# Kernel tuning notes

Measured on AMD Instinct MI355X. Metric: run time of the kernel, lower is better.

The kernel has to match this reference:

```python
import jax, jax.numpy as jnp
import numpy as np

T, G, D = 64, 1024, 128      # timesteps, detections per timestep, feature dim
N = T * G                    # total points; output rows = 3 + D = 131 cols


def setup_inputs() -> dict:
    key = jax.random.key(0)
    k1, k2 = jax.random.split(key)
    # time column: T distinct timestamps, G detections each (already time-sorted)
    times = jnp.repeat(jnp.arange(T, dtype=jnp.float32), G)
    xy = jax.random.uniform(k1, (N, 2), dtype=jnp.float32) * 128.0
    coor = jnp.concatenate([times[:, None], xy], axis=1)          # [N, 3]
    features = jax.random.normal(k2, (N, D), dtype=jnp.float32)   # [N, 128]
    return {"coor": coor, "features": features, "min_length": 8}


def _traverse(nxt):
    """Greedy chain building with a visited set (faithful to the torch loop).
    nxt[i] = precomputed best cosine match of point i in the next time group
    (-1 if i is in the last group). Returns (out_nodes, cid, clen):
      out_nodes[p] = node emitted at output slot p (all N slots filled),
      cid[p]       = chain id of slot p,
      clen[c]      = length of chain c.
    """
    def chain_cond(carry):
        visited, out, cid, p, cur, length, c = carry
        nx = nxt[cur]
        return (nx >= 0) & (~visited[nx])

    def chain_body(carry):
        visited, out, cid, p, cur, length, c = carry
        nx = nxt[cur]
        visited = visited.at[nx].set(True)
        out = out.at[p].set(nx)
        cid = cid.at[p].set(c)
        return (visited, out, cid, p + 1, nx, length + 1, c)

    def start_chain(st, start):
        visited, out, cid, clen, p, c = st
        visited = visited.at[start].set(True)
        out = out.at[p].set(start)
        cid = cid.at[p].set(c)
        carry = (visited, out, cid, p + 1, start, jnp.int32(1), c)
        visited, out, cid, p, cur, length, _ = jax.lax.while_loop(
            chain_cond, chain_body, carry)
        clen = clen.at[c].set(length)
        return (visited, out, cid, clen, p, c + 1)

    def body(start, st):
        start = jnp.int32(start)
        return jax.lax.cond(st[0][start], lambda s: s,
                            lambda s: start_chain(s, start), st)

    init = (jnp.zeros(N, bool),
            jnp.full(N, -1, jnp.int32),
            jnp.zeros(N, jnp.int32),
            jnp.zeros(N, jnp.int32),
            jnp.int32(0), jnp.int32(0))
    visited, out, cid, clen, p, c = jax.lax.fori_loop(0, N, body, init)
    return out, cid, clen


def reference(coor, features, min_length):
    # sort all points by time (stable; input is already time-sorted)
    order = jnp.argsort(coor[:, 0], stable=True)
    coor = coor[order]
    features = features[order]

    # --- vectorized precompute of the greedy next-match graph ---
    # group points by timestamp: [T, G, D]
    f = features.reshape(T, G, D)
    fn = f / jnp.maximum(jnp.linalg.norm(f, axis=-1, keepdims=True), 1e-6)
    # cosine sims between each time group and the next one: [T-1, G, G]
    sims = jnp.einsum('tgd,thd->tgh', fn[:-1], fn[1:])
    best = jnp.argmax(sims, axis=-1).astype(jnp.int32)        # [T-1, G]
    nxt = jnp.concatenate([
        (jnp.arange(1, T, dtype=jnp.int32)[:, None] * G + best).reshape(-1),
        jnp.full((G,), -1, jnp.int32)])                        # [N]
    nxt = jax.lax.stop_gradient(nxt)

    # --- sequential greedy traversal with visited set ---
    out_nodes, cid, clen = _traverse(nxt)

    # rows = [coor || features] in trajectory order
    rows = jnp.concatenate([coor, features], axis=1)[out_nodes]  # [N, 3+D]
    keep = clen[cid] >= min_length
    # pack kept rows to the top (order preserved), zero-pad the rest
    perm = jnp.argsort(~keep, stable=True)
    return jnp.where(keep[perm][:, None], rows[perm], 0.0)       # [N, 131]
```

## Files before the change

### kernel.cpp

```cpp
#include <hip/hip_runtime.h>
#include <hip/hip_bf16.h>
#include <hip/hip_fp16.h>

#define TT 64
#define GN 1024
#define DK 128
#define NN (TT * GN)
#define OUTC 131
#define TAU 5e-3f
#define CHUNK 64

typedef _Float16 f16x8 __attribute__((ext_vector_type(8)));
typedef float    f32x4 __attribute__((ext_vector_type(4)));

__device__ __forceinline__ unsigned f2h(float f) {
    return (unsigned)__half_as_ushort(__float2half(f));
}

__device__ __forceinline__ void gload_lds16(const void* g, void* l) {
    __builtin_amdgcn_global_load_lds(
        (const __attribute__((address_space(1))) unsigned int*)g,
        (__attribute__((address_space(3))) unsigned int*)l, 16, 0, 0);
}

__global__ void kconv(const float* __restrict__ feat, unsigned* __restrict__ fh,
                      float* __restrict__ rnf, double* __restrict__ rnd,
                      int* __restrict__ rcnt, int* __restrict__ clen) {
    if (blockIdx.x == 0 && threadIdx.x < 63) rcnt[threadIdx.x] = 0;
    if (blockIdx.x < 256) clen[blockIdx.x * 256 + threadIdx.x] = 0;
    int row  = blockIdx.x * 4 + (threadIdx.x >> 6);
    int lane = threadIdx.x & 63;
    const float* fr = feat + (size_t)row * DK;
    float2 v = *(const float2*)(fr + lane * 2);
    fh[(size_t)row * 64 + lane] = f2h(v.x) | (f2h(v.y) << 16);
    double s = (double)v.x * (double)v.x + (double)v.y * (double)v.y;
    #pragma unroll
    for (int off = 32; off > 0; off >>= 1)
        s += __shfl_down(s, off);
    if (lane == 0) {
        double m = sqrt(s);
        if (m < 1e-6) m = 1e-6;
        double r = 1.0 / m;
        rnd[row] = r;
        rnf[row] = (float)r;
    }
}

__global__ __launch_bounds__(256) void ksim(const unsigned* __restrict__ fh,
                                            const float* __restrict__ rnf,
                                            unsigned short* __restrict__ nxt16,
                                            int* __restrict__ rcnt,
                                            int* __restrict__ rlistT) {
    __shared__ int Tiles[2][8192];

    int id = blockIdx.x;
    int t  = id >> 3;
    int mt = id & 7;

    int tid  = threadIdx.x;
    int wave = tid >> 6;
    int lane = tid & 63;
    int la = lane & 15;
    int lq = lane >> 4;
    int wr = (wave & 1) * 64;
    int wc = (wave >> 1) * 64;

    const int* Ag = (const int*)fh + ((size_t)t * GN + mt * 128) * 64;
    const int* Bg = (const int*)fh + (size_t)(t + 1) * GN * 64;

    #pragma unroll
    for (int i = 0; i < 8; ++i) {
        int L = i * 256 + tid;
        int row = L >> 4, colG = (L & 15) ^ (row & 7);
        gload_lds16(Bg + row * 64 + colG * 4, &Tiles[0][L * 4]);
    }

    f16x8 af[4][4];
    #pragma unroll
    for (int kc = 0; kc < 4; ++kc)
        #pragma unroll
        for (int x = 0; x < 4; ++x)
            af[kc][x] = __builtin_bit_cast(f16x8,
                *(const int4*)&Ag[(wr + x * 16 + la) * 64 + (kc * 4 + lq) * 4]);

    float t1[4], t2[4]; int i1[4];
    #pragma unroll
    for (int s = 0; s < 4; ++s) { t1[s] = -3.4e38f; t2[s] = -3.4e38f; i1[s] = 0x7fffffff; }

    const float* rB = rnf + (size_t)(t + 1) * GN;
    __syncthreads();

    #pragma unroll 2
    for (int ntb = 0; ntb < 8; ++ntb) {
        int cur = ntb & 1;
        if (ntb < 7) {
            const int* Bn = Bg + (ntb + 1) * 128 * 64;
            int* dst = Tiles[cur ^ 1];
            #pragma unroll
            for (int i = 0; i < 8; ++i) {
                int L = i * 256 + tid;
                int row = L >> 4, colG = (L & 15) ^ (row & 7);
                gload_lds16(Bn + row * 64 + colG * 4, &dst[L * 4]);
            }
        }

        f32x4 acc[4][4];
        #pragma unroll
        for (int at = 0; at < 4; ++at)
            #pragma unroll
            for (int ct = 0; ct < 4; ++ct) acc[at][ct] = (f32x4){0.f, 0.f, 0.f, 0.f};

        const int* Bt = Tiles[cur];
        #pragma unroll
        for (int kc = 0; kc < 4; ++kc) {
            int sw = ((kc * 4 + lq) ^ (la & 7)) << 2;
            f16x8 bf[4];
            #pragma unroll
            for (int x = 0; x < 4; ++x)
                bf[x] = __builtin_bit_cast(f16x8, *(const int4*)&Bt[(wc + x * 16 + la) * 64 + sw]);
            #pragma unroll
            for (int at = 0; at < 4; ++at)
                #pragma unroll
                for (int ct = 0; ct < 4; ++ct)
                    acc[at][ct] = __builtin_amdgcn_mfma_f32_16x16x32_f16(
                        bf[ct], af[kc][at], acc[at][ct], 0, 0, 0);
        }

        #pragma unroll
        for (int ct = 0; ct < 4; ++ct) {
            float4 rnv = *(const float4*)&rB[ntb * 128 + wc + ct * 16 + lq * 4];
            int nbase = ntb * 128 + wc + ct * 16 + lq * 4;
            float rn[4] = {rnv.x, rnv.y, rnv.z, rnv.w};
            #pragma unroll
            for (int at = 0; at < 4; ++at) {
                #pragma unroll
                for (int reg = 0; reg < 4; ++reg) {
                    float v = acc[at][ct][reg] * rn[reg];
                    t2[at] = fmaxf(t2[at], fminf(v, t1[at]));
                    if (v > t1[at]) { t1[at] = v; i1[at] = nbase + reg; }
                }
            }
        }
        __syncthreads();
    }

    #pragma unroll
    for (int m = 16; m <= 32; m <<= 1) {
        #pragma unroll
        for (int s = 0; s < 4; ++s) {
            float o1 = __shfl_xor(t1[s], m);
            float o2 = __shfl_xor(t2[s], m);
            int   oi = __shfl_xor(i1[s], m);
            bool take = (o1 > t1[s]) || (o1 == t1[s] && oi < i1[s]);
            float nt2 = take ? fmaxf(o2, t1[s]) : fmaxf(t2[s], o1);
            if (take) { t1[s] = o1; i1[s] = oi; }
            t2[s] = nt2;
        }
    }

    float* mv1 = (float*)Tiles[0];
    float* mv2 = mv1 + 256;
    int*   mi1 = (int*)(mv2 + 256);
    if (lq == 0) {
        #pragma unroll
        for (int s = 0; s < 4; ++s) {
            int row = wr + s * 16 + la;
            int idx = row * 2 + (wave >> 1);
            mv1[idx] = t1[s]; mv2[idx] = t2[s]; mi1[idx] = i1[s];
        }
    }
    __syncthreads();

    if (tid < 128) {
        float best = mv1[tid * 2], sec, bw2 = mv2[tid * 2];
        int bi = mi1[tid * 2];
        float v1 = mv1[tid * 2 + 1], v2 = mv2[tid * 2 + 1];
        int  ii = mi1[tid * 2 + 1];
        if (v1 > best || (v1 == best && ii < bi)) {
            sec = fmaxf(best, v2); best = v1; bi = ii;
        } else {
            sec = fmaxf(v1, bw2);
        }
        int grow = mt * 128 + tid;
        if (best - sec < TAU) {
            int p = atomicAdd(&rcnt[t], 1);
            rlistT[t * 1024 + p] = grow;
        } else {
            nxt16[t * GN + grow] = (unsigned short)bi;
        }
    }
}

#define ACC4(sv, aa, bb)                                   \
    sv = fma((double)(aa).x, (double)(bb).x, sv);          \
    sv = fma((double)(aa).y, (double)(bb).y, sv);          \
    sv = fma((double)(aa).z, (double)(bb).z, sv);          \
    sv = fma((double)(aa).w, (double)(bb).w, sv);

__global__ __launch_bounds__(256) void krescue(const float* __restrict__ feat,
                                               const double* __restrict__ rnd,
                                               const int* __restrict__ rcnt,
                                               const int* __restrict__ rlistT,
                                               double* __restrict__ pbv,
                                               int* __restrict__ pbi) {
    __shared__ float  arows[CHUNK][128];
    __shared__ int    rl[CHUNK];
    __shared__ double cv[4][128];
    __shared__ int    ci[4][128];
    __shared__ double resv[CHUNK];
    __shared__ int    resi[CHUNK];
    int bid = blockIdx.x;
    int t = bid >> 2, q = bid & 3;
    int nr = rcnt[t];
    if (nr == 0) return;
    int tid  = threadIdx.x;
    int wave = tid >> 6, lane = tid & 63;
    int row  = tid >> 1;
    int par  = tid & 1;
    int h0 = q * 256 + row;
    int h1 = h0 + 128;

    const float* B0 = feat + ((size_t)(t + 1) * GN + h0) * DK + par * 64;
    const float* B1 = feat + ((size_t)(t + 1) * GN + h1) * DK + par * 64;
    float4 br0[16], br1[16];
    #pragma unroll
    for (int i = 0; i < 16; ++i) {
        br0[i] = *(const float4*)(B0 + i * 4);
        br1[i] = *(const float4*)(B1 + i * 4);
    }
    double rb0 = rnd[(t + 1) * GN + h0];
    double rb1 = rnd[(t + 1) * GN + h1];

    for (int c0 = 0; c0 < nr; c0 += CHUNK) {
        int cn = min(CHUNK, nr - c0);
        if (tid < cn) rl[tid] = rlistT[t * 1024 + c0 + tid];
        __syncthreads();
        for (int e = tid; e < cn * 32; e += 256) {
            int r = e >> 5, k = e & 31;
            *(float4*)&arows[r][k * 4] =
                *(const float4*)(feat + ((size_t)t * GN + rl[r]) * DK + k * 4);
        }
        __syncthreads();

        for (int rb = 0; rb < cn; rb += 4) {
            int rn4 = min(4, cn - rb);
            for (int rr = 0; rr < rn4; ++rr) {
                const float* ap = &arows[rb + rr][par * 64];
                double s0=0.0,s1=0.0,s2=0.0,s3=0.0;
                double u0=0.0,u1=0.0,u2=0.0,u3=0.0;
                #pragma unroll
                for (int i = 0; i < 16; i += 4) {
                    float4 a0 = *(const float4*)(ap + i * 4);
                    float4 a1 = *(const float4*)(ap + i * 4 + 4);
                    float4 a2 = *(const float4*)(ap + i * 4 + 8);
                    float4 a3 = *(const float4*)(ap + i * 4 + 12);
                    ACC4(s0, a0, br0[i])     ACC4(s1, a1, br0[i + 1])
                    ACC4(s2, a2, br0[i + 2]) ACC4(s3, a3, br0[i + 3])
                    ACC4(u0, a0, br1[i])     ACC4(u1, a1, br1[i + 1])
                    ACC4(u2, a2, br1[i + 2]) ACC4(u3, a3, br1[i + 3])
                }
                double s = (s0 + s1) + (s2 + s3);
                double u = (u0 + u1) + (u2 + u3);
                double so = __shfl_xor(s, 1);
                double uo = __shfl_xor(u, 1);
                if (par == 0) {
                    double v0 = (s + so) * rb0;
                    double v1 = (u + uo) * rb1;
                    if (v1 > v0) { cv[rr][row] = v1; ci[rr][row] = h1; }
                    else         { cv[rr][row] = v0; ci[rr][row] = h0; }
                }
            }
            __syncthreads();
            if (wave < rn4) {
                double v1 = cv[wave][lane];      int i1 = ci[wave][lane];
                double v2 = cv[wave][lane + 64]; int i2 = ci[wave][lane + 64];
                if (v2 > v1 || (v2 == v1 && i2 < i1)) { v1 = v2; i1 = i2; }
                #pragma unroll
                for (int off = 32; off > 0; off >>= 1) {
                    double ov = __shfl_down(v1, off);
                    int    oi = __shfl_down(i1, off);
                    if (ov > v1 || (ov == v1 && oi < i1)) { v1 = ov; i1 = oi; }
                }
                if (lane == 0) { resv[rb + wave] = v1; resi[rb + wave] = i1; }
            }
            __syncthreads();
        }

        if (tid < cn) {
            pbv[(size_t)bid * 1024 + c0 + tid] = resv[tid];
            pbi[(size_t)bid * 1024 + c0 + tid] = resi[tid];
        }
        __syncthreads();
    }
}

__global__ __launch_bounds__(1024) void kgraph(const unsigned short* __restrict__ nxt16,
                                               const int* __restrict__ rcnt,
                                               const int* __restrict__ rlistT,
                                               const double* __restrict__ pbv,
                                               const int* __restrict__ pbi,
                                               int* __restrict__ chain_of) {
    __shared__ unsigned short ns[64 * 1024];
    __shared__ int winner[2 * GN];
    __shared__ int rc[64];
    int g = threadIdx.x;

    #pragma unroll
    for (int i = 0; i < 8; ++i)
        gload_lds16((const char*)nxt16 + ((size_t)i * 1024 + g) * 16,
                    (char*)ns + ((size_t)i * 1024 + g) * 16);

    if (g < 63) rc[g] = rcnt[g];
    winner[g] = 0x7fffffff;
    chain_of[g] = g;
    __syncthreads();

    int t0 = g >> 4;
    if (t0 < TT - 1) {
        for (int ri = g & 15; ri < rc[t0]; ri += 16) {
            double bv = -1e300; int bi = 0x7fffffff;
            #pragma unroll
            for (int q = 0; q < 4; ++q) {
                double v  = pbv[(size_t)(t0 * 4 + q) * 1024 + ri];
                int    ii = pbi[(size_t)(t0 * 4 + q) * 1024 + ri];
                if (v > bv || (v == bv && ii < bi)) { bv = v; bi = ii; }
            }
            ns[t0 * GN + rlistT[t0 * 1024 + ri]] = (unsigned short)bi;
        }
    }
    __syncthreads();

    int mychain = g;
    for (int t = 0; t < TT - 1; ++t) {
        int* Wa = winner + (t & 1) * GN;
        int* Wb = winner + ((t + 1) & 1) * GN;
        int j = ns[t * GN + g];
        atomicMin(&Wa[j], mychain);
        Wb[g] = 0x7fffffff;
        __syncthreads();
        int w = Wa[g];
        mychain = (w == 0x7fffffff) ? (((t + 1) << 10) | g) : w;
        ns[t * GN + g] = (unsigned short)mychain;
        __syncthreads();
    }

    for (int t = 0; t < TT - 1; ++t)
        chain_of[(t + 1) * GN + g] = ns[t * GN + g];
}

__global__ void kclen(const int* __restrict__ chain_of, int* __restrict__ clen) {
    int i = blockIdx.x * 256 + threadIdx.x;
    atomicAdd(&clen[chain_of[i]], 1);
}

__global__ __launch_bounds__(1024) void kseg(const int* __restrict__ chain_of,
                                             const int* __restrict__ clen,
                                             const int* __restrict__ minp,
                                             int* __restrict__ oloc,
                                             int* __restrict__ partial) {
    __shared__ int ps[1024];
    int b = blockIdx.x, tid = threadIdx.x;
    int i = b * 1024 + tid;
    int ml = *minp;
    int cl = clen[i];
    int v = (chain_of[i] == i && cl >= ml) ? cl : 0;
    ps[tid] = v;
    __syncthreads();
    for (int off = 1; off < 1024; off <<= 1) {
        int add = (tid >= off) ? ps[tid - off] : 0;
        __syncthreads();
        ps[tid] += add;
        __syncthreads();
    }
    oloc[i] = ps[tid] - v;
    if (tid == 1023) partial[b] = ps[tid];
}

__global__ __launch_bounds__(256) void kout(const float* __restrict__ coor,
                                            const float* __restrict__ feat,
                                            const int* __restrict__ chain_of,
                                            const int* __restrict__ clen,
                                            const int* __restrict__ oloc,
                                            const int* __restrict__ partial,
                                            const int* __restrict__ minp,
                                            float* __restrict__ out) {
    __shared__ int pb[64];
    __shared__ int stot;
    int tid = threadIdx.x;
    if (tid < 64) {
        int v = partial[tid];
        int acc = v;
        #pragma unroll
        for (int off = 1; off < 64; off <<= 1) {
            int o = __shfl_up(acc, off);
            if (tid >= off) acc += o;
        }
        pb[tid] = acc - v;
        if (tid == 63) stot = acc;
    }
    __syncthreads();

    int node = blockIdx.x * 4 + (tid >> 6);
    int lane = tid & 63;
    int s = chain_of[node];
    if (clen[s] >= *minp) {
        int row = oloc[s] + pb[s >> 10] + (node >> 10) - (s >> 10);
        float* orow = out + (size_t)row * OUTC;
        const float* f = feat + (size_t)node * DK;
        if (lane < 3) orow[lane] = coor[(size_t)node * 3 + lane];
        orow[3 + lane]  = f[lane];
        orow[67 + lane] = f[64 + lane];
    }

    int zrow = stot + blockIdx.x * 4 + (tid >> 6);
    if (zrow < NN) {
        float* orow = out + (size_t)zrow * OUTC;
        orow[lane] = 0.f;
        orow[64 + lane] = 0.f;
        if (lane < 3) orow[128 + lane] = 0.f;
    }
}

extern "C" void kernel_launch(void* const* d_in, const int* in_sizes, int n_in,
                              void* d_out, int out_size, void* d_ws, size_t ws_size,
                              hipStream_t stream) {
    const float* coor   = (const float*)d_in[0];
    const float* feat   = (const float*)d_in[1];
    const int*   minlen = (const int*)d_in[2];
    float*       out    = (float*)d_out;

    char* ws = (char*)d_ws;
    double*         rnd      = (double*)(ws);
    float*          rnf      = (float*)(ws + 524288);
    unsigned short* nxt16    = (unsigned short*)(ws + 786432);
    int*            chain_of = (int*)(ws + 917504);
    int*            clen     = (int*)(ws + 1179648);
    int*            oloc     = (int*)(ws + 1441792);
    int*            rcnt     = (int*)(ws + 1703936);
    int*            partial  = (int*)(ws + 1704192);
    int*            rlistT   = (int*)(ws + 1705216);
    unsigned*       fh       = (unsigned*)(ws + 2097152);
    double*         pbv      = (double*)(ws + 18874368);
    int*            pbi      = (int*)(ws + 18874368 + 2064384);

    kconv<<<NN / 4, 256, 0, stream>>>(feat, fh, rnf, rnd, rcnt, clen);

    ksim<<<63 * 8, 256, 0, stream>>>(fh, rnf, nxt16, rcnt, rlistT);

    krescue<<<63 * 4, 256, 0, stream>>>(feat, rnd, rcnt, rlistT, pbv, pbi);

    kgraph<<<1, GN, 0, stream>>>(nxt16, rcnt, rlistT, pbv, pbi, chain_of);
    kclen<<<NN / 256, 256, 0, stream>>>(chain_of, clen);
    kseg<<<64, 1024, 0, stream>>>(chain_of, clen, minlen, oloc, partial);
    kout<<<NN / 4, 256, 0, stream>>>(coor, feat, chain_of, clen, oloc, partial,
                                     minlen, out);
}
```

Baseline: 228.3 us.

## Rescue ambiguous argmax rows using per-slice top-2 candidates instead of full fp64 rescan

The fp16 similarity kernel now keeps top-2 values and indices per lane slice and writes them to a workspace buffer. The rescue kernel uses these to re-score only candidates within the tolerance in fp64, one wave per ambiguous row. It falls back to a full slice scan only when a slice's second-best is also within the tolerance, so it no longer recomputes full fp64 rows against all 1024 next-group points. Rescued indices are written directly into nxt16, which drops the partial-result merge step from the single-block graph kernel. The cost is extra per-element select work in the similarity loop and a large strided candidate write.

```diff
diff --git a/kernel.cpp b/kernel.cpp
--- a/kernel.cpp
+++ b/kernel.cpp
@@ -8,7 +8,6 @@
 #define NN (TT * GN)
 #define OUTC 131
 #define TAU 5e-3f
-#define CHUNK 64
 
 typedef _Float16 f16x8 __attribute__((ext_vector_type(8)));
 typedef float    f32x4 __attribute__((ext_vector_type(4)));
@@ -50,7 +49,8 @@
                                             const float* __restrict__ rnf,
                                             unsigned short* __restrict__ nxt16,
                                             int* __restrict__ rcnt,
-                                            int* __restrict__ rlistT) {
+                                            int* __restrict__ rlistT,
+                                            float4* __restrict__ skt) {
     __shared__ int Tiles[2][8192];
 
     int id = blockIdx.x;
@@ -83,9 +83,11 @@
             af[kc][x] = __builtin_bit_cast(f16x8,
                 *(const int4*)&Ag[(wr + x * 16 + la) * 64 + (kc * 4 + lq) * 4]);
 
-    float t1[4], t2[4]; int i1[4];
-    #pragma unroll
-    for (int s = 0; s < 4; ++s) { t1[s] = -3.4e38f; t2[s] = -3.4e38f; i1[s] = 0x7fffffff; }
+    float t1[4], t2[4]; int i1[4], i2[4];
+    #pragma unroll
+    for (int s = 0; s < 4; ++s) {
+        t1[s] = -3.4e38f; t2[s] = -3.4e38f; i1[s] = 0x7fffffff; i2[s] = 0x7fffffff;
+    }
 
     const float* rB = rnf + (size_t)(t + 1) * GN;
     __syncthreads();
@@ -136,12 +138,27 @@
                 #pragma unroll
                 for (int reg = 0; reg < 4; ++reg) {
                     float v = acc[at][ct][reg] * rn[reg];
-                    t2[at] = fmaxf(t2[at], fminf(v, t1[at]));
-                    if (v > t1[at]) { t1[at] = v; i1[at] = nbase + reg; }
+                    int  nb = nbase + reg;
+                    bool gt1 = v > t1[at];
+                    bool gt2 = v > t2[at];
+                    t2[at] = gt1 ? t1[at] : (gt2 ? v  : t2[at]);
+                    i2[at] = gt1 ? i1[at] : (gt2 ? nb : i2[at]);
+                    t1[at] = gt1 ? v  : t1[at];
+                    i1[at] = gt1 ? nb : i1[at];
                 }
             }
         }
         __syncthreads();
+    }
+
+    {
+        float4* sko = skt + (size_t)((wave >> 1) * 4 + lq) * (63 * GN)
+                          + (size_t)t * GN + mt * 128;
+        #pragma unroll
+        for (int s = 0; s < 4; ++s)
+            sko[wr + s * 16 + la] = make_float4(t1[s], t2[s],
+                                                __int_as_float(i1[s]),
+                                                __int_as_float(i2[s]));
     }
 
     #pragma unroll
@@ -191,118 +208,75 @@
     }
 }
 
-#define ACC4(sv, aa, bb)                                   \
-    sv = fma((double)(aa).x, (double)(bb).x, sv);          \
-    sv = fma((double)(aa).y, (double)(bb).y, sv);          \
-    sv = fma((double)(aa).z, (double)(bb).z, sv);          \
-    sv = fma((double)(aa).w, (double)(bb).w, sv);
-
 __global__ __launch_bounds__(256) void krescue(const float* __restrict__ feat,
                                                const double* __restrict__ rnd,
                                                const int* __restrict__ rcnt,
                                                const int* __restrict__ rlistT,
-                                               double* __restrict__ pbv,
-                                               int* __restrict__ pbi) {
-    __shared__ float  arows[CHUNK][128];
-    __shared__ int    rl[CHUNK];
-    __shared__ double cv[4][128];
-    __shared__ int    ci[4][128];
-    __shared__ double resv[CHUNK];
-    __shared__ int    resi[CHUNK];
+                                               const float4* __restrict__ skt,
+                                               unsigned short* __restrict__ nxt16) {
     int bid = blockIdx.x;
-    int t = bid >> 2, q = bid & 3;
+    int t = bid >> 2;
     int nr = rcnt[t];
     if (nr == 0) return;
     int tid  = threadIdx.x;
     int wave = tid >> 6, lane = tid & 63;
-    int row  = tid >> 1;
-    int par  = tid & 1;
-    int h0 = q * 256 + row;
-    int h1 = h0 + 128;
-
-    const float* B0 = feat + ((size_t)(t + 1) * GN + h0) * DK + par * 64;
-    const float* B1 = feat + ((size_t)(t + 1) * GN + h1) * DK + par * 64;
-    float4 br0[16], br1[16];
-    #pragma unroll
-    for (int i = 0; i < 16; ++i) {
-        br0[i] = *(const float4*)(B0 + i * 4);
-        br1[i] = *(const float4*)(B1 + i * 4);
-    }
-    double rb0 = rnd[(t + 1) * GN + h0];
-    double rb1 = rnd[(t + 1) * GN + h1];
-
-    for (int c0 = 0; c0 < nr; c0 += CHUNK) {
-        int cn = min(CHUNK, nr - c0);
-        if (tid < cn) rl[tid] = rlistT[t * 1024 + c0 + tid];
-        __syncthreads();
-        for (int e = tid; e < cn * 32; e += 256) {
-            int r = e >> 5, k = e & 31;
-            *(float4*)&arows[r][k * 4] =
-                *(const float4*)(feat + ((size_t)t * GN + rl[r]) * DK + k * 4);
-        }
-        __syncthreads();
-
-        for (int rb = 0; rb < cn; rb += 4) {
-            int rn4 = min(4, cn - rb);
-            for (int rr = 0; rr < rn4; ++rr) {
-                const float* ap = &arows[rb + rr][par * 64];
-                double s0=0.0,s1=0.0,s2=0.0,s3=0.0;
-                double u0=0.0,u1=0.0,u2=0.0,u3=0.0;
+    int wk = (bid & 3) * 4 + wave;
+
+    const float*  Bt = feat + (size_t)(t + 1) * GN * DK;
+    const double* rb = rnd + (size_t)(t + 1) * GN;
+
+    for (int ri = wk; ri < nr; ri += 16) {
+        int arow = rlistT[t * 1024 + ri];
+        const float* ar = feat + ((size_t)t * GN + arow) * DK;
+        double a0 = (double)ar[lane * 2];
+        double a1 = (double)ar[lane * 2 + 1];
+
+        size_t gb = (size_t)t * GN + arow;
+        float4 e[8];
+        #pragma unroll
+        for (int s = 0; s < 8; ++s) e[s] = skt[(size_t)s * (63 * GN) + gb];
+        float best = e[0].x;
+        #pragma unroll
+        for (int s = 1; s < 8; ++s) best = fmaxf(best, e[s].x);
+        float thr = best - TAU;
+
+        double bv = -1.0e300; int bi = 0x7fffffff;
+        #pragma unroll
+        for (int s = 0; s < 8; ++s) {
+            if (e[s].x >= thr) {
+                int c = __float_as_int(e[s].z);
+                double d = fma(a0, (double)Bt[(size_t)c * DK + lane * 2],
+                               a1 * (double)Bt[(size_t)c * DK + lane * 2 + 1]);
                 #pragma unroll
-                for (int i = 0; i < 16; i += 4) {
-                    float4 a0 = *(const float4*)(ap + i * 4);
-                    float4 a1 = *(const float4*)(ap + i * 4 + 4);
-                    float4 a2 = *(const float4*)(ap + i * 4 + 8);
-                    float4 a3 = *(const float4*)(ap + i * 4 + 12);
-                    ACC4(s0, a0, br0[i])     ACC4(s1, a1, br0[i + 1])
-                    ACC4(s2, a2, br0[i + 2]) ACC4(s3, a3, br0[i + 3])
-                    ACC4(u0, a0, br1[i])     ACC4(u1, a1, br1[i + 1])
-                    ACC4(u2, a2, br1[i + 2]) ACC4(u3, a3, br1[i + 3])
-                }
-                double s = (s0 + s1) + (s2 + s3);
-                double u = (u0 + u1) + (u2 + u3);
-                double so = __shfl_xor(s, 1);
-                double uo = __shfl_xor(u, 1);
-                if (par == 0) {
-                    double v0 = (s + so) * rb0;
-                    double v1 = (u + uo) * rb1;
-                    if (v1 > v0) { cv[rr][row] = v1; ci[rr][row] = h1; }
-                    else         { cv[rr][row] = v0; ci[rr][row] = h0; }
+                for (int m = 1; m < 64; m <<= 1) d += __shfl_xor(d, m);
+                double v = d * rb[c];
+                if (v > bv || (v == bv && c < bi)) { bv = v; bi = c; }
+            }
+            if (e[s].y >= thr) {
+                int ch = s >> 2, lqs = s & 3;
+                for (int blk = 0; blk < 32; ++blk) {
+                    int cb = (blk >> 2) * 128 + ch * 64 + (blk & 3) * 16 + lqs * 4;
+                    #pragma unroll
+                    for (int reg = 0; reg < 4; ++reg) {
+                        int c = cb + reg;
+                        double d = fma(a0, (double)Bt[(size_t)c * DK + lane * 2],
+                                       a1 * (double)Bt[(size_t)c * DK + lane * 2 + 1]);
+                        #pragma unroll
+                        for (int m = 1; m < 64; m <<= 1) d += __shfl_xor(d, m);
+                        double v = d * rb[c];
+                        if (v > bv || (v == bv && c < bi)) { bv = v; bi = c; }
+                    }
                 }
             }
-            __syncthreads();
-            if (wave < rn4) {
-                double v1 = cv[wave][lane];      int i1 = ci[wave][lane];
-                double v2 = cv[wave][lane + 64]; int i2 = ci[wave][lane + 64];
-                if (v2 > v1 || (v2 == v1 && i2 < i1)) { v1 = v2; i1 = i2; }
-                #pragma unroll
-                for (int off = 32; off > 0; off >>= 1) {
-                    double ov = __shfl_down(v1, off);
-                    int    oi = __shfl_down(i1, off);
-                    if (ov > v1 || (ov == v1 && oi < i1)) { v1 = ov; i1 = oi; }
-                }
-                if (lane == 0) { resv[rb + wave] = v1; resi[rb + wave] = i1; }
-            }
-            __syncthreads();
-        }
-
-        if (tid < cn) {
-            pbv[(size_t)bid * 1024 + c0 + tid] = resv[tid];
-            pbi[(size_t)bid * 1024 + c0 + tid] = resi[tid];
-        }
-        __syncthreads();
+        }
+        if (lane == 0) nxt16[t * GN + arow] = (unsigned short)bi;
     }
 }
 
 __global__ __launch_bounds__(1024) void kgraph(const unsigned short* __restrict__ nxt16,
-                                               const int* __restrict__ rcnt,
-                                               const int* __restrict__ rlistT,
-                                               const double* __restrict__ pbv,
-                                               const int* __restrict__ pbi,
                                                int* __restrict__ chain_of) {
     __shared__ unsigned short ns[64 * 1024];
     __shared__ int winner[2 * GN];
-    __shared__ int rc[64];
     int g = threadIdx.x;
 
     #pragma unroll
@@ -310,24 +284,8 @@
         gload_lds16((const char*)nxt16 + ((size_t)i * 1024 + g) * 16,
                     (char*)ns + ((size_t)i * 1024 + g) * 16);
 
-    if (g < 63) rc[g] = rcnt[g];
     winner[g] = 0x7fffffff;
     chain_of[g] = g;
-    __syncthreads();
-
-    int t0 = g >> 4;
-    if (t0 < TT - 1) {
-        for (int ri = g & 15; ri < rc[t0]; ri += 16) {
-            double bv = -1e300; int bi = 0x7fffffff;
-            #pragma unroll
-            for (int q = 0; q < 4; ++q) {
-                double v  = pbv[(size_t)(t0 * 4 + q) * 1024 + ri];
-                int    ii = pbi[(size_t)(t0 * 4 + q) * 1024 + ri];
-                if (v > bv || (v == bv && ii < bi)) { bv = v; bi = ii; }
-            }
-            ns[t0 * GN + rlistT[t0 * 1024 + ri]] = (unsigned short)bi;
-        }
-    }
     __syncthreads();
 
     int mychain = g;
@@ -440,16 +398,15 @@
     int*            partial  = (int*)(ws + 1704192);
     int*            rlistT   = (int*)(ws + 1705216);
     unsigned*       fh       = (unsigned*)(ws + 2097152);
-    double*         pbv      = (double*)(ws + 18874368);
-    int*            pbi      = (int*)(ws + 18874368 + 2064384);
+    float4*         skt      = (float4*)(ws + 18874368);
 
     kconv<<<NN / 4, 256, 0, stream>>>(feat, fh, rnf, rnd, rcnt, clen);
 
-    ksim<<<63 * 8, 256, 0, stream>>>(fh, rnf, nxt16, rcnt, rlistT);
-
-    krescue<<<63 * 4, 256, 0, stream>>>(feat, rnd, rcnt, rlistT, pbv, pbi);
-
-    kgraph<<<1, GN, 0, stream>>>(nxt16, rcnt, rlistT, pbv, pbi, chain_of);
+    ksim<<<63 * 8, 256, 0, stream>>>(fh, rnf, nxt16, rcnt, rlistT, skt);
+
+    krescue<<<63 * 4, 256, 0, stream>>>(feat, rnd, rcnt, rlistT, skt, nxt16);
+
+    kgraph<<<1, GN, 0, stream>>>(nxt16, chain_of);
     kclen<<<NN / 256, 256, 0, stream>>>(chain_of, clen);
     kseg<<<64, 1024, 0, stream>>>(chain_of, clen, minlen, oloc, partial);
     kout<<<NN / 4, 256, 0, stream>>>(coor, feat, chain_of, clen, oloc, partial,
```

Result: slower. 318.7 us (+39.6%).
